# Performance work log

Hardware: AMD Instinct MI355X
Metric: run time of the kernel (lower is better)

## Reference

```python
import jax, jax.numpy as jnp
import numpy as np

X, U, AD, H = 32, 8, 24, 256
T, B = 128, 256
MIN_V, MAX_V = 0.01, 1.0
EPS = 1e-6


def setup_inputs() -> dict:
    key = jax.random.key(0)
    ks = jax.random.split(key, 10)
    s = lambda k, sh: jax.random.normal(k, sh, jnp.float32) * 0.05
    return {
        "u": jax.random.normal(ks[0], (T, B, U), jnp.float32),
        "a": jax.random.normal(ks[1], (T, B, AD), jnp.float32),
        "W1": s(ks[2], (H, X)), "b1": jnp.zeros((H,), jnp.float32),
        "W2": s(ks[3], (H, H)), "b2": jnp.zeros((H,), jnp.float32),
        "WA": s(ks[4], (X * X, H)), "bA": jnp.zeros((X * X,), jnp.float32),
        "WB": s(ks[5], (X * U, H)), "bB": jnp.zeros((X * U,), jnp.float32),
        "WC": s(ks[6], (AD * X, H)), "bC": jnp.zeros((AD * X,), jnp.float32),
        "Wnx": s(ks[7], (X, H)), "bnx": jnp.zeros((X,), jnp.float32),
        "Wna": s(ks[8], (AD, H)), "bna": jnp.zeros((AD,), jnp.float32),
        "alpha": jnp.array([0.01], jnp.float32),
    }


def _forward(u, a, W1, b1, W2, b2, WA, bA, WB, bB, WC, bC, Wnx, bnx, Wna, bna, alpha):
    eyeX = jnp.eye(X, dtype=u.dtype)
    eyeA = jnp.eye(AD, dtype=u.dtype)

    def dyn(x):
        # locally-linear dynamics heads; x: [B, X]
        h = jax.nn.relu(x @ W1.T + b1)
        h = jax.nn.relu(h @ W2.T + b2)
        b = x.shape[0]
        Am = eyeX + alpha[0] * (h @ WA.T + bA).reshape(b, X, X)
        Bm = (h @ WB.T + bB).reshape(b, X, U)
        Cm = (h @ WC.T + bC).reshape(b, AD, X)
        nx = MIN_V + (MAX_V - MIN_V) * jax.nn.sigmoid(h @ Wnx.T + bnx)
        na = MIN_V + (MAX_V - MIN_V) * jax.nn.sigmoid(h @ Wna.T + bna)
        return Am, Bm, Cm, nx, na

    def make_psd(P):
        return 0.5 * (P + jnp.swapaxes(P, -1, -2)) + EPS * eyeX

    def prior_step(mean, cov, u_t):
        Am, Bm, _, nx, _ = dyn(mean)
        nm = jnp.einsum('bij,bj->bi', Am, mean) + jnp.einsum('bij,bj->bi', Bm, u_t)
        nc = jnp.einsum('bij,bjk,blk->bil', Am, cov, Am) + nx[:, :, None] * eyeX
        return nm, make_psd(nc)

    def post_step(mean, cov, a_t):
        _, _, Cm, _, na = dyn(mean)
        S = jnp.einsum('bij,bjk,blk->bil', Cm, cov, Cm) + na[:, :, None] * eyeA
        Sp = jnp.linalg.pinv(S)
        G = jnp.einsum('bij,bkj,bkl->bil', cov, Cm, Sp)  # cov @ C^T @ pinv(S)
        innov = a_t - jnp.einsum('bij,bj->bi', Cm, mean)
        nm = mean + jnp.einsum('bij,bj->bi', G, innov)
        nc = cov - jnp.einsum('bij,bjk,bkl->bil', G, Cm, cov)
        return nm, make_psd(nc)

    pm0 = jnp.zeros((B, X), u.dtype)
    pc0 = jnp.broadcast_to(eyeX, (B, X, X))
    qm0, qc0 = post_step(pm0, pc0, a[0])

    def step(carry, inp):
        qm, qc = carry
        u_t, a_next = inp
        prm, prc = prior_step(qm, qc, u_t)
        nqm, nqc = post_step(prm, prc, a_next)
        return (nqm, nqc), (prm, prc, nqm, nqc)

    _, (prm, prc, qm, qc) = jax.lax.scan(step, (qm0, qc0), (u[:-1], a[1:]))
    prior_means = jnp.concatenate([pm0[None], prm], axis=0)
    prior_covs = jnp.concatenate([pc0[None], prc], axis=0)
    post_means = jnp.concatenate([qm0[None], qm], axis=0)
    post_covs = jnp.concatenate([qc0[None], qc], axis=0)
    return prior_means, prior_covs, post_means, post_covs


def reference(u, a, W1, b1, W2, b2, WA, bA, WB, bB, WC, bC, Wnx, bnx, Wna, bna, alpha):
    return _forward(u, a, W1, b1, W2, b2, WA, bA, WB, bB, WC, bC, Wnx, bnx, Wna, bna, alpha)
```

## Files before the change

kernel.cpp:

```cpp
#include <hip/hip_runtime.h>
#include <hip/hip_bf16.h>
#include <math.h>

typedef unsigned int uint32;
typedef _Float16 h2_t __attribute__((ext_vector_type(2)));

static constexpr int NX = 32;
static constexpr int NU = 8;
static constexpr int NA = 24;
static constexpr int NH = 256;
static constexpr int NT = 128;
static constexpr int NB = 256;
static constexpr int NXP = NX + 1;
static constexpr float MINV = 0.01f, MAXV = 1.0f, EPSV = 1e-6f;

static constexpr int H1O = NX*NX + NX*NU + NX;
static constexpr int H1P = 1344;
static constexpr int H2O = NA*NX + NA;
static constexpr int H2P = 800;

static constexpr size_t OFF_W1 = 0;
static constexpr size_t OFF_W2 = 4096;
static constexpr size_t OFF_H1 = OFF_W2 + 32768;
static constexpr size_t OFF_H2 = OFF_H1 + 172032;
static constexpr size_t OFF_B1 = OFF_H2 + 102400;
static constexpr size_t OFF_B2 = OFF_B1 + 1344;

__global__ void pack_half_off(const float* __restrict__ src, uint32* __restrict__ dst,
                              int O, int K, int LDP, int off)
{
    int idx = blockIdx.x * blockDim.x + threadIdx.x;
    int K2 = K >> 1;
    if (idx >= O * K2) return;
    int kk = idx % K2;
    int o  = idx / K2;
    int k  = kk * 2;
    int k8 = k >> 3, q = (k >> 1) & 3;
    _Float16 a = (_Float16)src[o * K + k];
    _Float16 b = (_Float16)src[o * K + k + 1];
    uint32 val = (uint32)__builtin_bit_cast(unsigned short, a)
               | ((uint32)__builtin_bit_cast(unsigned short, b) << 16);
    dst[((size_t)k8 * LDP + off + o) * 4 + q] = val;
}

__global__ void pack_bias3(const float* __restrict__ s0, int n0,
                           const float* __restrict__ s1, int n1,
                           const float* __restrict__ s2, int n2,
                           float* __restrict__ dst)
{
    int i = blockIdx.x * blockDim.x + threadIdx.x;
    if (i < n0) dst[i] = s0[i];
    else if (i < n0 + n1) dst[i] = s1[i - n0];
    else if (i < n0 + n1 + n2) dst[i] = s2[i - n0 - n1];
}

__device__ __forceinline__ float dot2(uint32 w, uint32 x, float acc)
{
#if __has_builtin(__builtin_amdgcn_fdot2)
    return __builtin_amdgcn_fdot2(__builtin_bit_cast(h2_t, w),
                                  __builtin_bit_cast(h2_t, x), acc, false);
#else
    h2_t a = __builtin_bit_cast(h2_t, w), b = __builtin_bit_cast(h2_t, x);
    return acc + (float)a[0] * (float)b[0] + (float)a[1] * (float)b[1];
#endif
}

__device__ __forceinline__ float dot8(uint4 w, uint4 x, float acc)
{
    acc = dot2(w.x, x.x, acc);
    acc = dot2(w.y, x.y, acc);
    acc = dot2(w.z, x.z, acc);
    acc = dot2(w.w, x.w, acc);
    return acc;
}

__device__ __forceinline__ void tri_decode(int p, int& l, int& i)
{
    int lo = (int)((sqrtf(8.f * (float)p + 1.f) - 1.f) * 0.5f);
    while ((lo + 1) * (lo + 2) / 2 <= p) lo++;
    while (lo * (lo + 1) / 2 > p) lo--;
    l = lo;
    i = p - lo * (lo + 1) / 2;
}

__device__ __forceinline__ float sigm_scaled(float z)
{
    return MINV + (MAXV - MINV) / (1.f + expf(-z));
}

__device__ __forceinline__ unsigned short f2h(float v)
{
    _Float16 h = (_Float16)v;
    return __builtin_bit_cast(unsigned short, h);
}

__device__ __forceinline__ void pack1_to(int tid, float v, uint32* d)
{
    unsigned short us = f2h(v);
    int pi = __shfl_xor((int)us, 1);
    if ((tid & 1) == 0)
        d[tid >> 1] = (uint32)us | ((uint32)pi << 16);
}

__global__ __launch_bounds__(1024, 4) void kf_kernel(
    const float* __restrict__ u, const float* __restrict__ a,
    const uint32* __restrict__ wsu,
    const float* __restrict__ b1, const float* __restrict__ b2,
    const float* __restrict__ alpha_p,
    float* __restrict__ out)
{
    const int tid = threadIdx.x;
    const int b   = blockIdx.x;
    const float alpha = alpha_p[0];

    const uint4* W1h = (const uint4*)(wsu + OFF_W1);
    const uint4* W2h = (const uint4*)(wsu + OFF_W2);
    const uint4* H1h = (const uint4*)(wsu + OFF_H1);
    const uint4* H2h = (const uint4*)(wsu + OFF_H2);
    const float* BH1 = (const float*)(wsu + OFF_B1);
    const float* BH2 = (const float*)(wsu + OFF_B2);

    __shared__ alignas(16) uint32 s_h1h[NH / 2];
    __shared__ alignas(16) uint32 s_h2h[NH / 2];
    __shared__ alignas(16) uint32 s_qmh[NX / 2];
    __shared__ alignas(16) uint32 s_pmh[NX / 2];
    __shared__ float s_part[4][NH];
    __shared__ float s_Am[NX * NXP];
    __shared__ float s_Bm[NX * NU];
    __shared__ float s_nx[NX];
    __shared__ float s_C[NA * NXP];
    __shared__ float s_na[NA];
    __shared__ float s_qm[NX], s_qc[NX * NXP];
    __shared__ float s_pm[NX], s_pc[NX * NXP];
    __shared__ float s_T2[NX * NXP];
    __shared__ float s_T1[NA * NXP];
    __shared__ float s_S[NA * NA];
    __shared__ float s_Y[NA * NX];
    __shared__ float s_innov[NA];
    __shared__ float s_a[NA], s_u[NU];

    const size_t pmO = 0;
    const size_t pcO = (size_t)NT * NB * NX;
    const size_t qmO = pcO + (size_t)NT * NB * NX * NX;
    const size_t qcO = qmO + (size_t)NT * NB * NX;

    int iT = 0, lT = 0;
    if (tid < 528) tri_decode(tid, lT, iT);
    int iS = 0, lS = 0;
    if (tid < 300) tri_decode(tid, lS, iS);

    for (int t = 0; t < NT; ++t) {
        const size_t mIdx = (size_t)t * NB + b;

        if (t == 0) {
            if (tid < NX) s_pm[tid] = 0.f;
            if (tid < NX / 2) s_pmh[tid] = 0u;
            {
                int i = tid >> 5, l = tid & 31;
                s_pc[i * NXP + l] = (i == l) ? 1.f : 0.f;
            }
            __syncthreads();
        } else {
            if (tid < NH) {
                const uint4* xh = (const uint4*)s_qmh;
                float acc = b1[tid];
                #pragma unroll
                for (int k8 = 0; k8 < 4; k8++)
                    acc = dot8(W1h[k8 * NH + tid], xh[k8], acc);
                pack1_to(tid, fmaxf(acc, 0.f), s_h1h);
            } else {
                const size_t mPrev = (size_t)(t - 1) * NB + b;
                for (int s = tid - 256; s < NX + NX * NX; s += 768) {
                    if (s < NX)
                        __builtin_nontemporal_store(s_qm[s], out + qmO + mPrev * NX + s);
                    else {
                        int o = s - NX, i = o >> 5, l = o & 31;
                        __builtin_nontemporal_store(s_qc[i * NXP + l],
                                                    out + qcO + mPrev * NX * NX + o);
                    }
                }
                if (tid >= 1016)
                    s_u[tid - 1016] = u[((size_t)(t - 1) * NB + b) * NU + (tid - 1016)];
            }
            __syncthreads();

            {
                int o = tid & 255, g = tid >> 8;
                const uint4* xh = (const uint4*)s_h1h;
                float acc = 0.f;
                #pragma unroll 4
                for (int k8 = g * 8; k8 < g * 8 + 8; k8++)
                    acc = dot8(W2h[k8 * NH + o], xh[k8], acc);
                s_part[g][o] = acc;
            }
            __syncthreads();

            if (tid < NH) {
                float v = fmaxf(s_part[0][tid] + s_part[1][tid] +
                                s_part[2][tid] + s_part[3][tid] + b2[tid], 0.f);
                pack1_to(tid, v, s_h2h);
            }
            __syncthreads();

            {
                const uint4* xh = (const uint4*)s_h2h;
                int o0 = tid, o1 = tid + 1024;
                float a0 = BH1[o0];
                float a1 = (o1 < H1O) ? BH1[o1] : 0.f;
                #pragma unroll 4
                for (int k8 = 0; k8 < 32; k8++) {
                    uint4 x = xh[k8];
                    a0 = dot8(H1h[k8 * H1P + o0], x, a0);
                    if (o1 < H1O) a1 = dot8(H1h[k8 * H1P + o1], x, a1);
                }
                {
                    int i = o0 >> 5, l = o0 & 31;
                    s_Am[i * NXP + l] = ((i == l) ? 1.f : 0.f) + alpha * a0;
                }
                if (o1 < H1O) {
                    if (o1 < NX * NX + NX * NU) s_Bm[o1 - NX * NX] = a1;
                    else s_nx[o1 - (NX * NX + NX * NU)] = sigm_scaled(a1);
                }
            }
            __syncthreads();

            {
                int i = tid >> 5, l = tid & 31;
                float acc = 0.f;
                #pragma unroll
                for (int j = 0; j < NX; j++)
                    acc = fmaf(s_Am[i * NXP + j], s_qc[j * NXP + l], acc);
                s_T2[i * NXP + l] = acc;
            }
            if (tid < NX) {
                float acc = 0.f;
                #pragma unroll
                for (int j = 0; j < NX; j++) acc = fmaf(s_Am[tid * NXP + j], s_qm[j], acc);
                #pragma unroll
                for (int j = 0; j < NU; j++) acc = fmaf(s_Bm[tid * NU + j], s_u[j], acc);
                s_pm[tid] = acc;
                pack1_to(tid, acc, s_pmh);
            }
            __syncthreads();

            if (tid < 528) {
                int i = iT, l = lT;
                float a_il = 0.f, a_li = 0.f;
                #pragma unroll
                for (int j = 0; j < NX; j++) {
                    a_il = fmaf(s_T2[i * NXP + j], s_Am[l * NXP + j], a_il);
                    a_li = fmaf(s_T2[l * NXP + j], s_Am[i * NXP + j], a_li);
                }
                if (i == l) {
                    s_pc[i * NXP + i] = a_il + s_nx[i] + EPSV;
                } else {
                    float v = 0.5f * (a_il + a_li);
                    s_pc[i * NXP + l] = v;
                    s_pc[l * NXP + i] = v;
                }
            }
            __syncthreads();
        }

        if (tid < NH) {
            const uint4* xh = (const uint4*)s_pmh;
            float acc = b1[tid];
            #pragma unroll
            for (int k8 = 0; k8 < 4; k8++)
                acc = dot8(W1h[k8 * NH + tid], xh[k8], acc);
            pack1_to(tid, fmaxf(acc, 0.f), s_h1h);
        } else {
            for (int s = tid - 256; s < NX + NX * NX; s += 768) {
                if (s < NX)
                    __builtin_nontemporal_store(s_pm[s], out + pmO + mIdx * NX + s);
                else {
                    int o = s - NX, i = o >> 5, l = o & 31;
                    __builtin_nontemporal_store(s_pc[i * NXP + l],
                                                out + pcO + mIdx * NX * NX + o);
                }
            }
            if (tid >= 1000)
                s_a[tid - 1000] = a[mIdx * NA + (tid - 1000)];
        }
        __syncthreads();

        {
            int o = tid & 255, g = tid >> 8;
            const uint4* xh = (const uint4*)s_h1h;
            float acc = 0.f;
            #pragma unroll 4
            for (int k8 = g * 8; k8 < g * 8 + 8; k8++)
                acc = dot8(W2h[k8 * NH + o], xh[k8], acc);
            s_part[g][o] = acc;
        }
        __syncthreads();

        if (tid < NH) {
            float v = fmaxf(s_part[0][tid] + s_part[1][tid] +
                            s_part[2][tid] + s_part[3][tid] + b2[tid], 0.f);
            pack1_to(tid, v, s_h2h);
        }
        __syncthreads();

        if (tid < H2P) {
            const uint4* xh = (const uint4*)s_h2h;
            float acc = BH2[tid];
            #pragma unroll 4
            for (int k8 = 0; k8 < 32; k8++)
                acc = dot8(H2h[k8 * H2P + tid], xh[k8], acc);
            if (tid < NA * NX) {
                int i = tid >> 5, l = tid & 31;
                s_C[i * NXP + l] = acc;
            } else if (tid < H2O) {
                s_na[tid - NA * NX] = sigm_scaled(acc);
            }
        }
        __syncthreads();

        if (tid < NA * NX) {
            int i = tid >> 5, l = tid & 31;
            float acc = 0.f;
            #pragma unroll
            for (int k = 0; k < NX; k++)
                acc = fmaf(s_C[i * NXP + k], s_pc[k * NXP + l], acc);
            s_T1[i * NXP + l] = acc;
        }
        if (tid >= 1000) {
            int i = tid - 1000;
            float acc = s_a[i];
            #pragma unroll
            for (int j = 0; j < NX; j++)
                acc = fmaf(-s_C[i * NXP + j], s_pm[j], acc);
            s_innov[i] = acc;
        }
        __syncthreads();

        if (tid < 300) {
            float acc = 0.f;
            #pragma unroll
            for (int j = 0; j < NX; j++)
                acc = fmaf(s_T1[iS * NXP + j], s_C[lS * NXP + j], acc);
            if (iS == lS) acc += s_na[iS];
            s_S[iS * NA + lS] = acc;
            s_S[lS * NA + iS] = acc;
        }
        __syncthreads();

        if (tid < 64) {
            const int j = tid;
            float r[NA];
            #pragma unroll
            for (int i = 0; i < NA; i++) {
                float v = 0.f;
                if (j < NA) v = s_S[i * NA + j];
                else if (j < NA + NX) v = s_T1[i * NXP + (j - NA)];
                r[i] = v;
            }
            #pragma unroll
            for (int k = 0; k < NA; k++) {
                float piv = __shfl(r[k], k);
                float ip = 1.0f / piv;
                r[k] *= ip;
                #pragma unroll
                for (int i = 0; i < NA; i++) {
                    if (i == k) continue;
                    float f = __shfl(r[i], k);
                    r[i] = fmaf(-f, r[k], r[i]);
                }
            }
            if (j >= NA && j < NA + NX) {
                #pragma unroll
                for (int i = 0; i < NA; i++) s_Y[i * NX + (j - NA)] = r[i];
            }
        }
        __syncthreads();

        if (tid < NX) {
            float acc = s_pm[tid];
            #pragma unroll
            for (int i = 0; i < NA; i++)
                acc = fmaf(s_Y[i * NX + tid], s_innov[i], acc);
            s_qm[tid] = acc;
            pack1_to(tid, acc, s_qmh);
        }
        if (tid < 528) {
            int i = iT, l = lT;
            float t_il = 0.f, t_li = 0.f;
            #pragma unroll
            for (int q = 0; q < NA; q++) {
                t_il = fmaf(s_Y[q * NX + i], s_T1[q * NXP + l], t_il);
                t_li = fmaf(s_Y[q * NX + l], s_T1[q * NXP + i], t_li);
            }
            if (i == l) {
                s_qc[i * NXP + i] = s_pc[i * NXP + i] - t_il + EPSV;
            } else {
                float v = 0.5f * ((s_pc[i * NXP + l] - t_il) + (s_pc[l * NXP + i] - t_li));
                s_qc[i * NXP + l] = v;
                s_qc[l * NXP + i] = v;
            }
        }
        __syncthreads();
    }

    {
        const size_t mLast = (size_t)(NT - 1) * NB + b;
        for (int s = tid; s < NX + NX * NX; s += 1024) {
            if (s < NX)
                __builtin_nontemporal_store(s_qm[s], out + qmO + mLast * NX + s);
            else {
                int o = s - NX, i = o >> 5, l = o & 31;
                __builtin_nontemporal_store(s_qc[i * NXP + l],
                                            out + qcO + mLast * NX * NX + o);
            }
        }
    }
}

extern "C" void kernel_launch(void* const* d_in, const int* in_sizes, int n_in,
                              void* d_out, int out_size, void* d_ws, size_t ws_size,
                              hipStream_t stream)
{
    const float* u    = (const float*)d_in[0];
    const float* a    = (const float*)d_in[1];
    const float* W1   = (const float*)d_in[2];
    const float* b1   = (const float*)d_in[3];
    const float* W2   = (const float*)d_in[4];
    const float* b2   = (const float*)d_in[5];
    const float* WA   = (const float*)d_in[6];
    const float* bA   = (const float*)d_in[7];
    const float* WB   = (const float*)d_in[8];
    const float* bB   = (const float*)d_in[9];
    const float* WC   = (const float*)d_in[10];
    const float* bC   = (const float*)d_in[11];
    const float* Wnx  = (const float*)d_in[12];
    const float* bnx  = (const float*)d_in[13];
    const float* Wna  = (const float*)d_in[14];
    const float* bna  = (const float*)d_in[15];
    const float* alph = (const float*)d_in[16];

    uint32* wsu = (uint32*)d_ws;
    float* out = (float*)d_out;

    auto pk = [&](const float* src, int O, int K, size_t dst_off, int LDP, int off) {
        int n = O * (K / 2);
        pack_half_off<<<(n + 255) / 256, 256, 0, stream>>>(src, wsu + dst_off, O, K, LDP, off);
    };
    pk(W1,  NH,      NX, OFF_W1, NH,  0);
    pk(W2,  NH,      NH, OFF_W2, NH,  0);
    pk(WA,  NX * NX, NH, OFF_H1, H1P, 0);
    pk(WB,  NX * NU, NH, OFF_H1, H1P, NX * NX);
    pk(Wnx, NX,      NH, OFF_H1, H1P, NX * NX + NX * NU);
    pk(WC,  NA * NX, NH, OFF_H2, H2P, 0);
    pk(Wna, NA,      NH, OFF_H2, H2P, NA * NX);

    pack_bias3<<<(H1O + 255) / 256, 256, 0, stream>>>(bA, NX * NX, bB, NX * NU, bnx, NX,
                                                      (float*)(wsu + OFF_B1));
    pack_bias3<<<(H2O + 255) / 256, 256, 0, stream>>>(bC, NA * NX, bna, NA, nullptr, 0,
                                                      (float*)(wsu + OFF_B2));

    kf_kernel<<<NB, 1024, 0, stream>>>(u, a, wsu, b1, b2, alph, out);
}
```

Baseline: 3.719 ms.

## Reschedule Kalman step stages to cut barriers and overlap work across phases

Reduces per-timestep barrier count by fusing the posterior covariance update into the next step's first MLP phase, folding the W2 partial-sum reduction into wave shuffles instead of shared memory, and computing the posterior mean inside the pinv wave. Output stores for covariances are moved to threads idle during the large head matvecs, and row padding changes to 34 so inner products can use float2 LDS loads. A lighter custom barrier replaces __syncthreads. Risks include bank conflicts from the even stride and correctness subtleties of the moved qc update and the custom barrier.

```diff
diff --git a/kernel.cpp b/kernel.cpp
--- a/kernel.cpp
+++ b/kernel.cpp
@@ -11,7 +11,7 @@
 static constexpr int NH = 256;
 static constexpr int NT = 128;
 static constexpr int NB = 256;
-static constexpr int NXP = NX + 1;
+static constexpr int NXP = 34;
 static constexpr float MINV = 0.01f, MAXV = 1.0f, EPSV = 1e-6f;
 
 static constexpr int H1O = NX*NX + NX*NU + NX;
@@ -102,6 +102,13 @@
         d[tid >> 1] = (uint32)us | ((uint32)pi << 16);
 }
 
+__device__ __forceinline__ void bar()
+{
+    asm volatile("s_waitcnt lgkmcnt(0)" ::: "memory");
+    __builtin_amdgcn_s_barrier();
+    asm volatile("" ::: "memory");
+}
+
 __global__ __launch_bounds__(1024, 4) void kf_kernel(
     const float* __restrict__ u, const float* __restrict__ a,
     const uint32* __restrict__ wsu,
@@ -124,16 +131,17 @@
     __shared__ alignas(16) uint32 s_h2h[NH / 2];
     __shared__ alignas(16) uint32 s_qmh[NX / 2];
     __shared__ alignas(16) uint32 s_pmh[NX / 2];
-    __shared__ float s_part[4][NH];
-    __shared__ float s_Am[NX * NXP];
+    __shared__ alignas(16) float s_Am[NX * NXP];
     __shared__ float s_Bm[NX * NU];
     __shared__ float s_nx[NX];
-    __shared__ float s_C[NA * NXP];
+    __shared__ alignas(16) float s_C[NA * NXP];
     __shared__ float s_na[NA];
-    __shared__ float s_qm[NX], s_qc[NX * NXP];
-    __shared__ float s_pm[NX], s_pc[NX * NXP];
-    __shared__ float s_T2[NX * NXP];
-    __shared__ float s_T1[NA * NXP];
+    __shared__ float s_qm[NX];
+    __shared__ alignas(16) float s_qc[NX * NXP];
+    __shared__ float s_pm[NX];
+    __shared__ alignas(16) float s_pc[NX * NXP];
+    __shared__ alignas(16) float s_T2[NX * NXP];
+    __shared__ alignas(16) float s_T1[NA * NXP];
     __shared__ float s_S[NA * NA];
     __shared__ float s_Y[NA * NX];
     __shared__ float s_innov[NA];
@@ -145,7 +153,7 @@
     const size_t qcO = qmO + (size_t)NT * NB * NX;
 
     int iT = 0, lT = 0;
-    if (tid < 528) tri_decode(tid, lT, iT);
+    if (tid >= 256 && tid < 784) tri_decode(tid - 256, lT, iT);
     int iS = 0, lS = 0;
     if (tid < 300) tri_decode(tid, lS, iS);
 
@@ -159,8 +167,10 @@
                 int i = tid >> 5, l = tid & 31;
                 s_pc[i * NXP + l] = (i == l) ? 1.f : 0.f;
             }
-            __syncthreads();
+            bar();
         } else {
+            const size_t mPrev = (size_t)(t - 1) * NB + b;
+
             if (tid < NH) {
                 const uint4* xh = (const uint4*)s_qmh;
                 float acc = b1[tid];
@@ -168,41 +178,50 @@
                 for (int k8 = 0; k8 < 4; k8++)
                     acc = dot8(W1h[k8 * NH + tid], xh[k8], acc);
                 pack1_to(tid, fmaxf(acc, 0.f), s_h1h);
-            } else {
-                const size_t mPrev = (size_t)(t - 1) * NB + b;
-                for (int s = tid - 256; s < NX + NX * NX; s += 768) {
-                    if (s < NX)
-                        __builtin_nontemporal_store(s_qm[s], out + qmO + mPrev * NX + s);
-                    else {
-                        int o = s - NX, i = o >> 5, l = o & 31;
-                        __builtin_nontemporal_store(s_qc[i * NXP + l],
-                                                    out + qcO + mPrev * NX * NX + o);
-                    }
-                }
-                if (tid >= 1016)
-                    s_u[tid - 1016] = u[((size_t)(t - 1) * NB + b) * NU + (tid - 1016)];
-            }
-            __syncthreads();
+            } else if (tid < 784) {
+                const int i = iT, l = lT;
+                float t_il = 0.f, t_li = 0.f;
+                #pragma unroll
+                for (int q = 0; q < NA; q++) {
+                    t_il = fmaf(s_Y[q * NX + i], s_T1[q * NXP + l], t_il);
+                    t_li = fmaf(s_Y[q * NX + l], s_T1[q * NXP + i], t_li);
+                }
+                if (i == l) {
+                    s_qc[i * NXP + i] = s_pc[i * NXP + i] - t_il + EPSV;
+                } else {
+                    float v = 0.5f * ((s_pc[i * NXP + l] - t_il) + (s_pc[l * NXP + i] - t_li));
+                    s_qc[i * NXP + l] = v;
+                    s_qc[l * NXP + i] = v;
+                }
+            } else if (tid < 816) {
+                __builtin_nontemporal_store(s_qm[tid - 784], out + qmO + mPrev * NX + (tid - 784));
+            } else if (tid < 824) {
+                s_u[tid - 816] = u[mPrev * NU + (tid - 816)];
+            }
+            bar();
 
             {
-                int o = tid & 255, g = tid >> 8;
+                int o = tid >> 2, g = tid & 3;
                 const uint4* xh = (const uint4*)s_h1h;
                 float acc = 0.f;
-                #pragma unroll 4
+                #pragma unroll
                 for (int k8 = g * 8; k8 < g * 8 + 8; k8++)
                     acc = dot8(W2h[k8 * NH + o], xh[k8], acc);
-                s_part[g][o] = acc;
-            }
-            __syncthreads();
-
-            if (tid < NH) {
-                float v = fmaxf(s_part[0][tid] + s_part[1][tid] +
-                                s_part[2][tid] + s_part[3][tid] + b2[tid], 0.f);
-                pack1_to(tid, v, s_h2h);
-            }
-            __syncthreads();
+                acc += __shfl_xor(acc, 1);
+                acc += __shfl_xor(acc, 2);
+                float v = fmaxf(acc + b2[o], 0.f);
+                unsigned short us = f2h(v);
+                int pi = __shfl_xor((int)us, 4);
+                if ((tid & 7) == 0) s_h2h[tid >> 3] = (uint32)us | ((uint32)pi << 16);
+            }
+            bar();
 
             {
+                if (tid >= 320) {
+                    for (int s = tid - 320; s < NX * NX; s += 704)
+                        __builtin_nontemporal_store(s_qc[(s >> 5) * NXP + (s & 31)],
+                                                    out + qcO + mPrev * NX * NX + s);
+                }
                 const uint4* xh = (const uint4*)s_h2h;
                 int o0 = tid, o1 = tid + 1024;
                 float a0 = BH1[o0];
@@ -222,14 +241,19 @@
                     else s_nx[o1 - (NX * NX + NX * NU)] = sigm_scaled(a1);
                 }
             }
-            __syncthreads();
+            bar();
 
             {
                 int i = tid >> 5, l = tid & 31;
+                const float2* amr = (const float2*)&s_Am[i * NXP];
+                const float2* qcr = (const float2*)&s_qc[l * NXP];
                 float acc = 0.f;
                 #pragma unroll
-                for (int j = 0; j < NX; j++)
-                    acc = fmaf(s_Am[i * NXP + j], s_qc[j * NXP + l], acc);
+                for (int j2 = 0; j2 < NX / 2; j2++) {
+                    float2 am = amr[j2], qc = qcr[j2];
+                    acc = fmaf(am.x, qc.x, acc);
+                    acc = fmaf(am.y, qc.y, acc);
+                }
                 s_T2[i * NXP + l] = acc;
             }
             if (tid < NX) {
@@ -241,15 +265,32 @@
                 s_pm[tid] = acc;
                 pack1_to(tid, acc, s_pmh);
             }
-            __syncthreads();
-
-            if (tid < 528) {
-                int i = iT, l = lT;
+            bar();
+        }
+
+        if (tid < NH) {
+            const uint4* xh = (const uint4*)s_pmh;
+            float acc = b1[tid];
+            #pragma unroll
+            for (int k8 = 0; k8 < 4; k8++)
+                acc = dot8(W1h[k8 * NH + tid], xh[k8], acc);
+            pack1_to(tid, fmaxf(acc, 0.f), s_h1h);
+        } else if (tid < 784) {
+            if (t > 0) {
+                const int i = iT, l = lT;
+                const float2* t2i = (const float2*)&s_T2[i * NXP];
+                const float2* t2l = (const float2*)&s_T2[l * NXP];
+                const float2* ami = (const float2*)&s_Am[i * NXP];
+                const float2* aml = (const float2*)&s_Am[l * NXP];
                 float a_il = 0.f, a_li = 0.f;
                 #pragma unroll
-                for (int j = 0; j < NX; j++) {
-                    a_il = fmaf(s_T2[i * NXP + j], s_Am[l * NXP + j], a_il);
-                    a_li = fmaf(s_T2[l * NXP + j], s_Am[i * NXP + j], a_li);
+                for (int j2 = 0; j2 < NX / 2; j2++) {
+                    float2 p = t2i[j2], q = aml[j2];
+                    a_il = fmaf(p.x, q.x, a_il);
+                    a_il = fmaf(p.y, q.y, a_il);
+                    float2 r2 = t2l[j2], s2 = ami[j2];
+                    a_li = fmaf(r2.x, s2.x, a_li);
+                    a_li = fmaf(r2.y, s2.y, a_li);
                 }
                 if (i == l) {
                     s_pc[i * NXP + i] = a_il + s_nx[i] + EPSV;
@@ -259,53 +300,33 @@
                     s_pc[l * NXP + i] = v;
                 }
             }
-            __syncthreads();
-        }
-
-        if (tid < NH) {
-            const uint4* xh = (const uint4*)s_pmh;
-            float acc = b1[tid];
-            #pragma unroll
-            for (int k8 = 0; k8 < 4; k8++)
-                acc = dot8(W1h[k8 * NH + tid], xh[k8], acc);
-            pack1_to(tid, fmaxf(acc, 0.f), s_h1h);
-        } else {
-            for (int s = tid - 256; s < NX + NX * NX; s += 768) {
-                if (s < NX)
-                    __builtin_nontemporal_store(s_pm[s], out + pmO + mIdx * NX + s);
-                else {
-                    int o = s - NX, i = o >> 5, l = o & 31;
-                    __builtin_nontemporal_store(s_pc[i * NXP + l],
-                                                out + pcO + mIdx * NX * NX + o);
-                }
-            }
-            if (tid >= 1000)
-                s_a[tid - 1000] = a[mIdx * NA + (tid - 1000)];
-        }
-        __syncthreads();
+        } else if (tid < 816) {
+            __builtin_nontemporal_store(s_pm[tid - 784], out + pmO + mIdx * NX + (tid - 784));
+        } else if (tid < 840) {
+            s_a[tid - 816] = a[mIdx * NA + (tid - 816)];
+        }
+        bar();
 
         {
-            int o = tid & 255, g = tid >> 8;
+            int o = tid >> 2, g = tid & 3;
             const uint4* xh = (const uint4*)s_h1h;
             float acc = 0.f;
-            #pragma unroll 4
+            #pragma unroll
             for (int k8 = g * 8; k8 < g * 8 + 8; k8++)
                 acc = dot8(W2h[k8 * NH + o], xh[k8], acc);
-            s_part[g][o] = acc;
-        }
-        __syncthreads();
-
-        if (tid < NH) {
-            float v = fmaxf(s_part[0][tid] + s_part[1][tid] +
-                            s_part[2][tid] + s_part[3][tid] + b2[tid], 0.f);
-            pack1_to(tid, v, s_h2h);
-        }
-        __syncthreads();
+            acc += __shfl_xor(acc, 1);
+            acc += __shfl_xor(acc, 2);
+            float v = fmaxf(acc + b2[o], 0.f);
+            unsigned short us = f2h(v);
+            int pi = __shfl_xor((int)us, 4);
+            if ((tid & 7) == 0) s_h2h[tid >> 3] = (uint32)us | ((uint32)pi << 16);
+        }
+        bar();
 
         if (tid < H2P) {
             const uint4* xh = (const uint4*)s_h2h;
             float acc = BH2[tid];
-            #pragma unroll 4
+            #pragma unroll 8
             for (int k8 = 0; k8 < 32; k8++)
                 acc = dot8(H2h[k8 * H2P + tid], xh[k8], acc);
             if (tid < NA * NX) {
@@ -314,37 +335,50 @@
             } else if (tid < H2O) {
                 s_na[tid - NA * NX] = sigm_scaled(acc);
             }
-        }
-        __syncthreads();
+        } else {
+            for (int s = tid - 800; s < NX * NX; s += 224)
+                __builtin_nontemporal_store(s_pc[(s >> 5) * NXP + (s & 31)],
+                                            out + pcO + mIdx * NX * NX + s);
+        }
+        bar();
 
         if (tid < NA * NX) {
             int i = tid >> 5, l = tid & 31;
+            const float2* cr = (const float2*)&s_C[i * NXP];
+            const float2* pr = (const float2*)&s_pc[l * NXP];
             float acc = 0.f;
             #pragma unroll
-            for (int k = 0; k < NX; k++)
-                acc = fmaf(s_C[i * NXP + k], s_pc[k * NXP + l], acc);
+            for (int k2 = 0; k2 < NX / 2; k2++) {
+                float2 c = cr[k2], p = pr[k2];
+                acc = fmaf(c.x, p.x, acc);
+                acc = fmaf(c.y, p.y, acc);
+            }
             s_T1[i * NXP + l] = acc;
-        }
-        if (tid >= 1000) {
-            int i = tid - 1000;
+        } else if (tid < NA * NX + NA) {
+            int i = tid - NA * NX;
             float acc = s_a[i];
             #pragma unroll
             for (int j = 0; j < NX; j++)
                 acc = fmaf(-s_C[i * NXP + j], s_pm[j], acc);
             s_innov[i] = acc;
         }
-        __syncthreads();
+        bar();
 
         if (tid < 300) {
+            const float2* t1 = (const float2*)&s_T1[iS * NXP];
+            const float2* cl = (const float2*)&s_C[lS * NXP];
             float acc = 0.f;
             #pragma unroll
-            for (int j = 0; j < NX; j++)
-                acc = fmaf(s_T1[iS * NXP + j], s_C[lS * NXP + j], acc);
+            for (int j2 = 0; j2 < NX / 2; j2++) {
+                float2 x = t1[j2], y = cl[j2];
+                acc = fmaf(x.x, y.x, acc);
+                acc = fmaf(x.y, y.y, acc);
+            }
             if (iS == lS) acc += s_na[iS];
             s_S[iS * NA + lS] = acc;
             s_S[lS * NA + iS] = acc;
         }
-        __syncthreads();
+        bar();
 
         if (tid < 64) {
             const int j = tid;
@@ -369,39 +403,39 @@
                 }
             }
             if (j >= NA && j < NA + NX) {
-                #pragma unroll
-                for (int i = 0; i < NA; i++) s_Y[i * NX + (j - NA)] = r[i];
-            }
-        }
-        __syncthreads();
-
-        if (tid < NX) {
-            float acc = s_pm[tid];
-            #pragma unroll
-            for (int i = 0; i < NA; i++)
-                acc = fmaf(s_Y[i * NX + tid], s_innov[i], acc);
-            s_qm[tid] = acc;
-            pack1_to(tid, acc, s_qmh);
-        }
-        if (tid < 528) {
-            int i = iT, l = lT;
-            float t_il = 0.f, t_li = 0.f;
-            #pragma unroll
-            for (int q = 0; q < NA; q++) {
-                t_il = fmaf(s_Y[q * NX + i], s_T1[q * NXP + l], t_il);
-                t_li = fmaf(s_Y[q * NX + l], s_T1[q * NXP + i], t_li);
-            }
-            if (i == l) {
-                s_qc[i * NXP + i] = s_pc[i * NXP + i] - t_il + EPSV;
-            } else {
-                float v = 0.5f * ((s_pc[i * NXP + l] - t_il) + (s_pc[l * NXP + i] - t_li));
-                s_qc[i * NXP + l] = v;
-                s_qc[l * NXP + i] = v;
-            }
-        }
-        __syncthreads();
+                const int x = j - NA;
+                float acc = s_pm[x];
+                #pragma unroll
+                for (int i = 0; i < NA; i++) {
+                    s_Y[i * NX + x] = r[i];
+                    acc = fmaf(r[i], s_innov[i], acc);
+                }
+                s_qm[x] = acc;
+                unsigned short us = f2h(acc);
+                int pi = __shfl_xor((int)us, 1);
+                if ((x & 1) == 0) s_qmh[x >> 1] = (uint32)us | ((uint32)pi << 16);
+            }
+        }
+        bar();
     }
 
+    if (tid >= 256 && tid < 784) {
+        const int i = iT, l = lT;
+        float t_il = 0.f, t_li = 0.f;
+        #pragma unroll
+        for (int q = 0; q < NA; q++) {
+            t_il = fmaf(s_Y[q * NX + i], s_T1[q * NXP + l], t_il);
+            t_li = fmaf(s_Y[q * NX + l], s_T1[q * NXP + i], t_li);
+        }
+        if (i == l) {
+            s_qc[i * NXP + i] = s_pc[i * NXP + i] - t_il + EPSV;
+        } else {
+            float v = 0.5f * ((s_pc[i * NXP + l] - t_il) + (s_pc[l * NXP + i] - t_li));
+            s_qc[i * NXP + l] = v;
+            s_qc[l * NXP + i] = v;
+        }
+    }
+    bar();
     {
         const size_t mLast = (size_t)(NT - 1) * NB + b;
         for (int s = tid; s < NX + NX * NX; s += 1024) {
```

Result: slower. 5.389 ms (+44.9%).
